# Performance work log

Hardware: AMD Instinct MI355X
Metric: run time of the kernel (lower is better)

## Reference

```python
import jax, jax.numpy as jnp
import numpy as np

DIM = 512
HEADS = 8
DIM_HEAD = 64
SCALE = DIM_HEAD ** -0.5


def setup_inputs() -> dict:
    key = jax.random.key(0)
    k1, k2, k3, k4, k5 = jax.random.split(key, 5)
    inner = HEADS * DIM_HEAD
    x = jax.random.normal(k1, (16, DIM, 32, 32), dtype=jnp.float32)
    W_proj = jax.random.normal(k2, (DIM, inner * 3), dtype=jnp.float32) * (DIM ** -0.5)
    b_proj = jax.random.normal(k3, (inner * 3,), dtype=jnp.float32) * 0.01
    W_out = jax.random.normal(k4, (inner, DIM), dtype=jnp.float32) * (inner ** -0.5)
    b_out = jax.random.normal(k5, (DIM,), dtype=jnp.float32) * 0.01
    return {"x": x, "W_proj": W_proj, "b_proj": b_proj, "W_out": W_out, "b_out": b_out}


def reference(x, W_proj, b_proj, W_out, b_out):
    b, c, hh, ww = x.shape
    s = hh * ww
    xs = x.reshape(b, c, s).transpose(0, 2, 1)  # b s c
    qkv = xs @ W_proj + b_proj                  # b s (heads * 3*dim_head)
    qkv = qkv.reshape(b, s, HEADS, 3 * DIM_HEAD)
    q, k, v = jnp.split(qkv, 3, axis=-1)        # each: b s h d
    w = jnp.einsum('bshd,bthd->bsth', q, k) * SCALE
    w = jax.nn.softmax(w, axis=2)
    res = jnp.einsum('bsth,bthd->bshd', w, v).reshape(b, s, HEADS * DIM_HEAD)
    out = res @ W_out + b_out + xs              # b s c (residual)
    return out.transpose(0, 2, 1).reshape(b, c, hh, ww)
```

## Files before the change

kernel.cpp:

```cpp
#include <hip/hip_runtime.h>
#include <hip/hip_bf16.h>

#define BATCH 16
#define CDIM  512
#define SEQ   1024
#define HEADS 8
#define DHEAD 64
#define N3    1536
#define QSCALE 0.18033688011112042f

typedef unsigned short ushort_t;
typedef __attribute__((ext_vector_type(8))) short short8;
typedef __attribute__((ext_vector_type(4))) float f32x4;

__device__ __forceinline__ unsigned f2bf(float f) {
    unsigned u = __float_as_uint(f);
    u += 0x7fffu + ((u >> 16) & 1u);
    return u >> 16;
}
__device__ __forceinline__ float fast_exp2(float x) {
    float r;
    asm("v_exp_f32 %0, %1" : "=v"(r) : "v"(x));
    return r;
}
__device__ __forceinline__ unsigned pack_bf16_trunc(float lo, float hi) {
    return __builtin_amdgcn_perm(__float_as_uint(hi), __float_as_uint(lo), 0x07060302u);
}
__device__ __forceinline__ void async16(const void* g, void* l) {
    __builtin_amdgcn_global_load_lds(
        (const __attribute__((address_space(1))) unsigned int*)g,
        (__attribute__((address_space(3))) unsigned int*)l, 16, 0, 0);
}
__device__ __forceinline__ void barrier_raw() {
    __builtin_amdgcn_sched_barrier(0);
    __builtin_amdgcn_s_barrier();
    __builtin_amdgcn_sched_barrier(0);
}
#define WAIT_VMCNT(n) asm volatile("s_waitcnt vmcnt(" #n ")" ::: "memory")


__global__ __launch_bounds__(256) void blockify_kernel(
    const float* __restrict__ in, ushort_t* __restrict__ out, int C)
{
    __shared__ float t[64][65];
    const int k0 = blockIdx.y * 64, c0 = blockIdx.x * 64;
    const float* inb = in + (size_t)blockIdx.z * 512 * C;
    const int tid = threadIdx.x;
#pragma unroll
    for (int i = 0; i < 16; ++i) {
        int idx = tid + i * 256;
        int r = idx >> 6, c = idx & 63;
        t[r][c] = inb[(size_t)(k0 + r) * C + c0 + c];
    }
    __syncthreads();
    const size_t mbase = (size_t)blockIdx.z * C + c0;
    const int ml = tid & 63;
#pragma unroll
    for (int i = 0; i < 2; ++i) {
        int oct = (tid >> 6) + i * 4;
        size_t m = mbase + ml;
        int mt = (int)(m >> 7), mr = (int)(m & 127);
        int m16 = mr >> 4, col = mr & 15;
        int k = k0 + oct * 8;
        int it = k >> 5, q = (k >> 3) & 3;
        uint4 pk;
        pk.x = f2bf(t[oct * 8 + 0][ml]) | (f2bf(t[oct * 8 + 1][ml]) << 16);
        pk.y = f2bf(t[oct * 8 + 2][ml]) | (f2bf(t[oct * 8 + 3][ml]) << 16);
        pk.z = f2bf(t[oct * 8 + 4][ml]) | (f2bf(t[oct * 8 + 5][ml]) << 16);
        pk.w = f2bf(t[oct * 8 + 6][ml]) | (f2bf(t[oct * 8 + 7][ml]) << 16);
        size_t off = ((size_t)(mt * 16 + it) * 8 + m16) * 512 + (q * 16 + col) * 8;
        *(uint4*)&out[off] = pk;
    }
}

__global__ __launch_bounds__(256) void qkv_gemm_kernel(
    const ushort_t* __restrict__ xtb, const ushort_t* __restrict__ WpTb,
    const float* __restrict__ bp,
    ushort_t* __restrict__ q_buf, ushort_t* __restrict__ kb,
    ushort_t* __restrict__ vb)
{
    __shared__ alignas(16) ushort_t Asub[2][8 * 512];
    __shared__ alignas(16) ushort_t Bsub[2][8 * 512];

    const int tid = threadIdx.x, w = tid >> 6, lane = tid & 63;
    const int quad = lane >> 4, col = lane & 15;
    const int wm = w >> 1, wn = w & 1;

    const int lin = blockIdx.x + 12 * blockIdx.y;
    const int xcd = lin & 7;
    const int rr  = lin >> 3;
    const int n0  = (rr % 12) * 128;
    const int m0  = ((rr / 12) * 8 + xcd) * 128;

    f32x4 acc[4][4];
#pragma unroll
    for (int i = 0; i < 4; ++i)
#pragma unroll
        for (int j = 0; j < 4; ++j) acc[i][j] = (f32x4){0.f, 0.f, 0.f, 0.f};

    const ushort_t* Ab = xtb  + (size_t)(m0 >> 7) * 65536 + (w * 2) * 512 + lane * 8;
    const ushort_t* Bb = WpTb + (size_t)(n0 >> 7) * 65536 + (w * 2) * 512 + lane * 8;

#define QKV_STAGE(buf, t)                                         \
    do {                                                          \
        async16(Ab + (t) * 4096,       &Asub[buf][(w * 2 + 0) * 512]); \
        async16(Ab + (t) * 4096 + 512, &Asub[buf][(w * 2 + 1) * 512]); \
        async16(Bb + (t) * 4096,       &Bsub[buf][(w * 2 + 0) * 512]); \
        async16(Bb + (t) * 4096 + 512, &Bsub[buf][(w * 2 + 1) * 512]); \
    } while (0)

    QKV_STAGE(0, 0);
    QKV_STAGE(1, 1);
    for (int it = 0; it < 16; ++it) {
        const int cur = it & 1;
        if (it < 15) { WAIT_VMCNT(4); } else { WAIT_VMCNT(0); }
        barrier_raw();

        short8 af[4], bfr[4];
#pragma unroll
        for (int i = 0; i < 4; ++i) af[i]  = *(const short8*)&Asub[cur][(wm * 4 + i) * 512 + lane * 8];
#pragma unroll
        for (int j = 0; j < 4; ++j) bfr[j] = *(const short8*)&Bsub[cur][(wn * 4 + j) * 512 + lane * 8];
#pragma unroll
        for (int i = 0; i < 4; ++i)
#pragma unroll
            for (int j = 0; j < 4; ++j)
                acc[i][j] = __builtin_amdgcn_mfma_f32_16x16x32_bf16(af[i], bfr[j], acc[i][j], 0, 0, 0);

        if (it < 14) {
            barrier_raw();
            QKV_STAGE(cur, it + 2);
        }
    }
#undef QKV_STAGE

    const int b = m0 >> 10, s0 = m0 & 1023;
    const size_t b8 = (size_t)b * HEADS;
#pragma unroll
    for (int j = 0; j < 4; ++j) {
        int nb = n0 + wn * 64 + j * 16;
        int h = nb / 192, rem = nb % 192;
        int type = rem >> 6, dbase = rem & 63;
        float bias = bp[nb + col];
        size_t bh = b8 + h;
        int d = dbase + col;
#pragma unroll
        for (int i = 0; i < 4; ++i) {
            int sb = s0 + wm * 64 + i * 16 + quad * 4;
            f32x4 v = acc[i][j];
            if (type == 2) {
                unsigned lo = f2bf(v[0] + bias) | (f2bf(v[1] + bias) << 16);
                unsigned hi = f2bf(v[2] + bias) | (f2bf(v[3] + bias) << 16);
                uint2 pk; pk.x = lo; pk.y = hi;
                int itv = sb >> 6, sub = (d >> 4) * 2 + ((sb >> 5) & 1);
                size_t off = ((bh * 16 + itv) * 8 + sub) * 512
                           + (((sb >> 2) & 3) * 16 + (d & 15)) * 8
                           + ((sb >> 4) & 1) * 4;
                *(uint2*)&vb[off] = pk;
            } else if (type == 1) {
#pragma unroll
                for (int r = 0; r < 4; ++r) {
                    int t = sb + r;
                    int itk = t >> 6, sub = ((t >> 4) & 3) * 2 + (d >> 5);
                    size_t off = ((bh * 16 + itk) * 8 + sub) * 512
                               + (((d >> 3) & 3) * 16 + (t & 15)) * 8 + (d & 7);
                    kb[off] = (ushort_t)f2bf(v[r] + bias);
                }
            } else {
#pragma unroll
                for (int r = 0; r < 4; ++r)
                    q_buf[(bh * SEQ + sb + r) * DHEAD + d] =
                        (ushort_t)f2bf((v[r] + bias) * QSCALE);
            }
        }
    }
}

__global__ __launch_bounds__(128) void attn_kernel(
    const ushort_t* __restrict__ q_buf, const ushort_t* __restrict__ kb,
    const ushort_t* __restrict__ vb, ushort_t* __restrict__ resb)
{
    __shared__ alignas(16) ushort_t Kf[2][8 * 512];
    __shared__ alignas(16) ushort_t Vf[2][8 * 512];

    const int tid  = threadIdx.x;
    const int w    = tid >> 6;
    const int lane = tid & 63;
    const int quad = lane >> 4;
    const int col  = lane & 15;

    const int bhid = blockIdx.x;
    const int b = bhid >> 3, h = bhid & 7;
    const int q0 = blockIdx.y * 128;
    const size_t bh = (size_t)b * HEADS + h;

    const ushort_t* qp = q_buf + ((bh * SEQ) + q0 + w * 64 + col) * DHEAD + quad * 8;
    short8 qf0[4], qf1[4];
#pragma unroll
    for (int g = 0; g < 4; ++g) {
        qf0[g] = *(const short8*)(qp + g * 16 * DHEAD);
        qf1[g] = *(const short8*)(qp + g * 16 * DHEAD + 32);
    }

    short8 ones;
#pragma unroll
    for (int i = 0; i < 8; ++i) ones[i] = (short)0x3F80;

    f32x4 O[4][4];
#pragma unroll
    for (int g = 0; g < 4; ++g)
#pragma unroll
        for (int i = 0; i < 4; ++i) O[g][i] = (f32x4){0.f, 0.f, 0.f, 0.f};
    f32x4 L[4];
#pragma unroll
    for (int g = 0; g < 4; ++g) L[g] = (f32x4){0.f, 0.f, 0.f, 0.f};

    const ushort_t* kaB = kb + (size_t)bh * 65536 + (w * 4) * 512 + lane * 8;
    const ushort_t* vaB = vb + (size_t)bh * 65536 + (w * 4) * 512 + lane * 8;

#define ATTN_STAGE(buf)                                            \
    do {                                                           \
        async16(kaB,        &Kf[buf][(w * 4 + 0) * 512]);          \
        async16(kaB + 512,  &Kf[buf][(w * 4 + 1) * 512]);          \
        async16(kaB + 1024, &Kf[buf][(w * 4 + 2) * 512]);          \
        async16(kaB + 1536, &Kf[buf][(w * 4 + 3) * 512]);          \
        async16(vaB,        &Vf[buf][(w * 4 + 0) * 512]);          \
        async16(vaB + 512,  &Vf[buf][(w * 4 + 1) * 512]);          \
        async16(vaB + 1024, &Vf[buf][(w * 4 + 2) * 512]);          \
        async16(vaB + 1536, &Vf[buf][(w * 4 + 3) * 512]);          \
        kaB += 4096;                                               \
        vaB += 4096;                                               \
    } while (0)

    ATTN_STAGE(0);

    for (int it = 0; it < 16; ++it) {
        const int cur = it & 1;
        const ushort_t* kc = Kf[cur];
        const ushort_t* vc = Vf[cur];
        __syncthreads();
        if (it < 15) ATTN_STAGE(cur ^ 1);

        short8 kf[8];
#pragma unroll
        for (int t16 = 0; t16 < 4; ++t16) {
            kf[2 * t16 + 0] = *(const short8*)&kc[(t16 * 2 + 0) * 512 + lane * 8];
            kf[2 * t16 + 1] = *(const short8*)&kc[(t16 * 2 + 1) * 512 + lane * 8];
        }

        short8 pf[4][2];
#pragma unroll
        for (int g = 0; g < 4; ++g) {
            f32x4 S[4];
            __builtin_amdgcn_s_setprio(1);
#pragma unroll
            for (int t16 = 0; t16 < 4; ++t16) {
                f32x4 a = (f32x4){0.f, 0.f, 0.f, 0.f};
                a = __builtin_amdgcn_mfma_f32_16x16x32_bf16(kf[2 * t16 + 0], qf0[g], a, 0, 0, 0);
                a = __builtin_amdgcn_mfma_f32_16x16x32_bf16(kf[2 * t16 + 1], qf1[g], a, 0, 0, 0);
                S[t16] = a;
            }
            __builtin_amdgcn_s_setprio(0);
            union { uint4 u; short8 s; } p0, p1;
            p0.u.x = pack_bf16_trunc(fast_exp2(S[0][0]), fast_exp2(S[0][1]));
            p0.u.y = pack_bf16_trunc(fast_exp2(S[0][2]), fast_exp2(S[0][3]));
            p0.u.z = pack_bf16_trunc(fast_exp2(S[1][0]), fast_exp2(S[1][1]));
            p0.u.w = pack_bf16_trunc(fast_exp2(S[1][2]), fast_exp2(S[1][3]));
            p1.u.x = pack_bf16_trunc(fast_exp2(S[2][0]), fast_exp2(S[2][1]));
            p1.u.y = pack_bf16_trunc(fast_exp2(S[2][2]), fast_exp2(S[2][3]));
            p1.u.z = pack_bf16_trunc(fast_exp2(S[3][0]), fast_exp2(S[3][1]));
            p1.u.w = pack_bf16_trunc(fast_exp2(S[3][2]), fast_exp2(S[3][3]));
            pf[g][0] = p0.s;
            pf[g][1] = p1.s;
        }

#pragma unroll
        for (int d16 = 0; d16 < 4; ++d16) {
            const short8 v0 = *(const short8*)&vc[(d16 * 2 + 0) * 512 + lane * 8];
            const short8 v1 = *(const short8*)&vc[(d16 * 2 + 1) * 512 + lane * 8];
            __builtin_amdgcn_s_setprio(1);
#pragma unroll
            for (int g = 0; g < 4; ++g) {
                O[g][d16] = __builtin_amdgcn_mfma_f32_16x16x32_bf16(pf[g][0], v0, O[g][d16], 0, 0, 0);
                O[g][d16] = __builtin_amdgcn_mfma_f32_16x16x32_bf16(pf[g][1], v1, O[g][d16], 0, 0, 0);
            }
            __builtin_amdgcn_s_setprio(0);
        }
#pragma unroll
        for (int g = 0; g < 4; ++g) {
            L[g] = __builtin_amdgcn_mfma_f32_16x16x32_bf16(pf[g][0], ones, L[g], 0, 0, 0);
            L[g] = __builtin_amdgcn_mfma_f32_16x16x32_bf16(pf[g][1], ones, L[g], 0, 0, 0);
        }
    }
#undef ATTN_STAGE

    const int mt = b * 8 + (q0 >> 7);
#pragma unroll
    for (int g = 0; g < 4; ++g) {
        const int m16 = w * 4 + g;
#pragma unroll
        for (int r = 0; r < 4; ++r) {
            float inv = 1.f / L[g][r];
            const int mcol = quad * 4 + r;
#pragma unroll
            for (int d16 = 0; d16 < 4; ++d16) {
                int itk = h * 2 + (d16 >> 1);
                int kq = (d16 & 1) * 2 + (col >> 3);
                size_t off = ((size_t)(mt * 16 + itk) * 8 + m16) * 512
                           + (kq * 16 + mcol) * 8 + (col & 7);
                resb[off] = (ushort_t)f2bf(O[g][d16][r] * inv);
            }
        }
    }
}

__global__ __launch_bounds__(256) void out_gemm_kernel(
    const ushort_t* __restrict__ resb, const ushort_t* __restrict__ WoTb,
    const float* __restrict__ bo, const float* __restrict__ x,
    float* __restrict__ out)
{
    __shared__ alignas(16) ushort_t SMEM[2 * 2 * 8 * 512];
    ushort_t (*Asub)[8 * 512] = (ushort_t (*)[8 * 512])(SMEM);
    ushort_t (*Bsub)[8 * 512] = (ushort_t (*)[8 * 512])(SMEM + 2 * 8 * 512);
    float* tb = (float*)SMEM;

    const int tid = threadIdx.x, w = tid >> 6, lane = tid & 63;
    const int quad = lane >> 4, col = lane & 15;
    const int wm = w >> 1, wn = w & 1;

    const int lin = blockIdx.x + 4 * blockIdx.y;
    const int xcd = lin & 7;
    const int rr  = lin >> 3;
    const int n0  = (rr & 3) * 128;
    const int m0  = ((rr >> 2) * 8 + xcd) * 128;

    f32x4 acc[4][4];
#pragma unroll
    for (int i = 0; i < 4; ++i)
#pragma unroll
        for (int j = 0; j < 4; ++j) acc[i][j] = (f32x4){0.f, 0.f, 0.f, 0.f};

    const ushort_t* Ab = resb + (size_t)(m0 >> 7) * 65536 + (w * 2) * 512 + lane * 8;
    const ushort_t* Bb = WoTb + (size_t)(n0 >> 7) * 65536 + (w * 2) * 512 + lane * 8;

#define OUT_STAGE(buf, t)                                         \
    do {                                                          \
        async16(Ab + (t) * 4096,       &Asub[buf][(w * 2 + 0) * 512]); \
        async16(Ab + (t) * 4096 + 512, &Asub[buf][(w * 2 + 1) * 512]); \
        async16(Bb + (t) * 4096,       &Bsub[buf][(w * 2 + 0) * 512]); \
        async16(Bb + (t) * 4096 + 512, &Bsub[buf][(w * 2 + 1) * 512]); \
    } while (0)

    OUT_STAGE(0, 0);
    OUT_STAGE(1, 1);
    for (int it = 0; it < 16; ++it) {
        const int cur = it & 1;
        if (it < 15) { WAIT_VMCNT(4); } else { WAIT_VMCNT(0); }
        barrier_raw();

        short8 af[4], bfr[4];
#pragma unroll
        for (int i = 0; i < 4; ++i) af[i]  = *(const short8*)&Asub[cur][(wm * 4 + i) * 512 + lane * 8];
#pragma unroll
        for (int j = 0; j < 4; ++j) bfr[j] = *(const short8*)&Bsub[cur][(wn * 4 + j) * 512 + lane * 8];
#pragma unroll
        for (int i = 0; i < 4; ++i)
#pragma unroll
            for (int j = 0; j < 4; ++j)
                acc[i][j] = __builtin_amdgcn_mfma_f32_16x16x32_bf16(af[i], bfr[j], acc[i][j], 0, 0, 0);

        if (it < 14) {
            barrier_raw();
            OUT_STAGE(cur, it + 2);
        }
    }
#undef OUT_STAGE

    const int b = m0 >> 10, s0 = m0 & 1023;
    const int half = lane >> 5, l32 = lane & 31;
#pragma unroll
    for (int j = 0; j < 4; ++j) {
        __syncthreads();
#pragma unroll
        for (int i = 0; i < 4; ++i) {
            f32x4 v = acc[i][j];
            float* dst = &tb[(wn * 16 + col) * 132 + wm * 64 + i * 16 + quad * 4];
            dst[0] = v[0]; dst[1] = v[1]; dst[2] = v[2]; dst[3] = v[3];
        }
        __syncthreads();
#pragma unroll
        for (int p = 0; p < 4; ++p) {
            int nl = w * 8 + p * 2 + half;
            int n = n0 + j * 16 + (nl & 15) + (nl >> 4) * 64;
            float4 t4 = *(const float4*)&tb[nl * 132 + l32 * 4];
            size_t o = ((size_t)b * CDIM + n) * SEQ + s0 + l32 * 4;
            float4 xr = *(const float4*)&x[o];
            float bias = bo[n];
            float4 ov;
            ov.x = t4.x + bias + xr.x;
            ov.y = t4.y + bias + xr.y;
            ov.z = t4.z + bias + xr.z;
            ov.w = t4.w + bias + xr.w;
            *(float4*)&out[o] = ov;
        }
    }
}

extern "C" void kernel_launch(void* const* d_in, const int* in_sizes, int n_in,
                              void* d_out, int out_size, void* d_ws, size_t ws_size,
                              hipStream_t stream) {
    const float* x  = (const float*)d_in[0];
    const float* Wp = (const float*)d_in[1];
    const float* bp = (const float*)d_in[2];
    const float* Wo = (const float*)d_in[3];
    const float* bo = (const float*)d_in[4];
    float* out = (float*)d_out;

    ushort_t* xtb   = (ushort_t*)d_ws;
    ushort_t* WpTb  = xtb   + (size_t)8388608;
    ushort_t* WoTb  = WpTb  + (size_t)786432;
    ushort_t* q_buf = WoTb  + (size_t)262144;
    ushort_t* kb    = q_buf + (size_t)8388608;
    ushort_t* vb    = kb    + (size_t)8388608;
    ushort_t* resb  = vb    + (size_t)8388608;

    blockify_kernel<<<dim3(16, 8, 16), 256, 0, stream>>>(x,  xtb,  1024);
    blockify_kernel<<<dim3(24, 8, 1),  256, 0, stream>>>(Wp, WpTb, 1536);
    blockify_kernel<<<dim3(8, 8, 1),   256, 0, stream>>>(Wo, WoTb, 512);
    qkv_gemm_kernel<<<dim3(12, 128), 256, 0, stream>>>(xtb, WpTb, bp, q_buf, kb, vb);
    attn_kernel<<<dim3(128, 8), 128, 0, stream>>>(q_buf, kb, vb, resb);
    out_gemm_kernel<<<dim3(4, 128), 256, 0, stream>>>(resb, WoTb, bo, x, out);
}
```

Baseline: 187.6 us.

## Merge blockify launches, vectorize loads, and use 2-wave QKV GEMM blocks

```diff
diff --git a/kernel.cpp b/kernel.cpp
--- a/kernel.cpp
+++ b/kernel.cpp
@@ -40,20 +40,32 @@
 
 
 __global__ __launch_bounds__(256) void blockify_kernel(
-    const float* __restrict__ in, ushort_t* __restrict__ out, int C)
+    const float* __restrict__ x, const float* __restrict__ Wp,
+    const float* __restrict__ Wo,
+    ushort_t* __restrict__ xtb, ushort_t* __restrict__ WpTb,
+    ushort_t* __restrict__ WoTb)
 {
-    __shared__ float t[64][65];
+    const int zz = blockIdx.z;
+    const float* in;
+    ushort_t* out;
+    int C, zbat;
+    if (zz < 16)       { if (blockIdx.x >= 16) return; in = x;  out = xtb;  C = 1024; zbat = zz; }
+    else if (zz == 16) {                               in = Wp; out = WpTb; C = 1536; zbat = 0;  }
+    else               { if (blockIdx.x >= 8)  return; in = Wo; out = WoTb; C = 512;  zbat = 0;  }
+
+    __shared__ float t[64][68];
     const int k0 = blockIdx.y * 64, c0 = blockIdx.x * 64;
-    const float* inb = in + (size_t)blockIdx.z * 512 * C;
+    const float* inb = in + (size_t)zbat * 512 * C;
     const int tid = threadIdx.x;
 #pragma unroll
-    for (int i = 0; i < 16; ++i) {
+    for (int i = 0; i < 4; ++i) {
         int idx = tid + i * 256;
-        int r = idx >> 6, c = idx & 63;
-        t[r][c] = inb[(size_t)(k0 + r) * C + c0 + c];
+        int r = idx >> 4, c4 = idx & 15;
+        float4 f = *(const float4*)&inb[(size_t)(k0 + r) * C + c0 + c4 * 4];
+        *(float4*)&t[r][c4 * 4] = f;
     }
     __syncthreads();
-    const size_t mbase = (size_t)blockIdx.z * C + c0;
+    const size_t mbase = (size_t)zbat * C + c0;
     const int ml = tid & 63;
 #pragma unroll
     for (int i = 0; i < 2; ++i) {
@@ -73,7 +85,7 @@
     }
 }
 
-__global__ __launch_bounds__(256) void qkv_gemm_kernel(
+__global__ __launch_bounds__(128) void qkv_gemm_kernel(
     const ushort_t* __restrict__ xtb, const ushort_t* __restrict__ WpTb,
     const float* __restrict__ bp,
     ushort_t* __restrict__ q_buf, ushort_t* __restrict__ kb,
@@ -84,7 +96,6 @@
 
     const int tid = threadIdx.x, w = tid >> 6, lane = tid & 63;
     const int quad = lane >> 4, col = lane & 15;
-    const int wm = w >> 1, wn = w & 1;
 
     const int lin = blockIdx.x + 12 * blockIdx.y;
     const int xcd = lin & 7;
@@ -92,39 +103,43 @@
     const int n0  = (rr % 12) * 128;
     const int m0  = ((rr / 12) * 8 + xcd) * 128;
 
-    f32x4 acc[4][4];
+    f32x4 acc[4][8];
 #pragma unroll
     for (int i = 0; i < 4; ++i)
 #pragma unroll
-        for (int j = 0; j < 4; ++j) acc[i][j] = (f32x4){0.f, 0.f, 0.f, 0.f};
-
-    const ushort_t* Ab = xtb  + (size_t)(m0 >> 7) * 65536 + (w * 2) * 512 + lane * 8;
-    const ushort_t* Bb = WpTb + (size_t)(n0 >> 7) * 65536 + (w * 2) * 512 + lane * 8;
-
-#define QKV_STAGE(buf, t)                                         \
-    do {                                                          \
-        async16(Ab + (t) * 4096,       &Asub[buf][(w * 2 + 0) * 512]); \
-        async16(Ab + (t) * 4096 + 512, &Asub[buf][(w * 2 + 1) * 512]); \
-        async16(Bb + (t) * 4096,       &Bsub[buf][(w * 2 + 0) * 512]); \
-        async16(Bb + (t) * 4096 + 512, &Bsub[buf][(w * 2 + 1) * 512]); \
+        for (int j = 0; j < 8; ++j) acc[i][j] = (f32x4){0.f, 0.f, 0.f, 0.f};
+
+    const ushort_t* Ab = xtb  + (size_t)(m0 >> 7) * 65536 + (w * 4) * 512 + lane * 8;
+    const ushort_t* Bb = WpTb + (size_t)(n0 >> 7) * 65536 + (w * 4) * 512 + lane * 8;
+
+#define QKV_STAGE(buf, t)                                              \
+    do {                                                               \
+        async16(Ab + (t) * 4096,        &Asub[buf][(w * 4 + 0) * 512]); \
+        async16(Ab + (t) * 4096 + 512,  &Asub[buf][(w * 4 + 1) * 512]); \
+        async16(Ab + (t) * 4096 + 1024, &Asub[buf][(w * 4 + 2) * 512]); \
+        async16(Ab + (t) * 4096 + 1536, &Asub[buf][(w * 4 + 3) * 512]); \
+        async16(Bb + (t) * 4096,        &Bsub[buf][(w * 4 + 0) * 512]); \
+        async16(Bb + (t) * 4096 + 512,  &Bsub[buf][(w * 4 + 1) * 512]); \
+        async16(Bb + (t) * 4096 + 1024, &Bsub[buf][(w * 4 + 2) * 512]); \
+        async16(Bb + (t) * 4096 + 1536, &Bsub[buf][(w * 4 + 3) * 512]); \
     } while (0)
 
     QKV_STAGE(0, 0);
     QKV_STAGE(1, 1);
     for (int it = 0; it < 16; ++it) {
         const int cur = it & 1;
-        if (it < 15) { WAIT_VMCNT(4); } else { WAIT_VMCNT(0); }
+        if (it < 15) { WAIT_VMCNT(8); } else { WAIT_VMCNT(0); }
         barrier_raw();
 
-        short8 af[4], bfr[4];
-#pragma unroll
-        for (int i = 0; i < 4; ++i) af[i]  = *(const short8*)&Asub[cur][(wm * 4 + i) * 512 + lane * 8];
-#pragma unroll
-        for (int j = 0; j < 4; ++j) bfr[j] = *(const short8*)&Bsub[cur][(wn * 4 + j) * 512 + lane * 8];
+        short8 af[4], bfr[8];
+#pragma unroll
+        for (int i = 0; i < 4; ++i) af[i]  = *(const short8*)&Asub[cur][(w * 4 + i) * 512 + lane * 8];
+#pragma unroll
+        for (int j = 0; j < 8; ++j) bfr[j] = *(const short8*)&Bsub[cur][j * 512 + lane * 8];
 #pragma unroll
         for (int i = 0; i < 4; ++i)
 #pragma unroll
-            for (int j = 0; j < 4; ++j)
+            for (int j = 0; j < 8; ++j)
                 acc[i][j] = __builtin_amdgcn_mfma_f32_16x16x32_bf16(af[i], bfr[j], acc[i][j], 0, 0, 0);
 
         if (it < 14) {
@@ -137,8 +152,8 @@
     const int b = m0 >> 10, s0 = m0 & 1023;
     const size_t b8 = (size_t)b * HEADS;
 #pragma unroll
-    for (int j = 0; j < 4; ++j) {
-        int nb = n0 + wn * 64 + j * 16;
+    for (int j = 0; j < 8; ++j) {
+        int nb = n0 + j * 16;
         int h = nb / 192, rem = nb % 192;
         int type = rem >> 6, dbase = rem & 63;
         float bias = bp[nb + col];
@@ -146,7 +161,7 @@
         int d = dbase + col;
 #pragma unroll
         for (int i = 0; i < 4; ++i) {
-            int sb = s0 + wm * 64 + i * 16 + quad * 4;
+            int sb = s0 + (w * 4 + i) * 16 + quad * 4;
             f32x4 v = acc[i][j];
             if (type == 2) {
                 unsigned lo = f2bf(v[0] + bias) | (f2bf(v[1] + bias) << 16);
@@ -424,10 +439,8 @@
     ushort_t* vb    = kb    + (size_t)8388608;
     ushort_t* resb  = vb    + (size_t)8388608;
 
-    blockify_kernel<<<dim3(16, 8, 16), 256, 0, stream>>>(x,  xtb,  1024);
-    blockify_kernel<<<dim3(24, 8, 1),  256, 0, stream>>>(Wp, WpTb, 1536);
-    blockify_kernel<<<dim3(8, 8, 1),   256, 0, stream>>>(Wo, WoTb, 512);
-    qkv_gemm_kernel<<<dim3(12, 128), 256, 0, stream>>>(xtb, WpTb, bp, q_buf, kb, vb);
+    blockify_kernel<<<dim3(24, 8, 18), 256, 0, stream>>>(x, Wp, Wo, xtb, WpTb, WoTb);
+    qkv_gemm_kernel<<<dim3(12, 128), 128, 0, stream>>>(xtb, WpTb, bp, q_buf, kb, vb);
     attn_kernel<<<dim3(128, 8), 128, 0, stream>>>(q_buf, kb, vb, resb);
     out_gemm_kernel<<<dim3(4, 128), 256, 0, stream>>>(resb, WoTb, bo, x, out);
 }
```

Result: slower. 213.0 us (+13.5%).
